# Kernel optimization log

Measured on AMD Instinct MI355X. Metric: run time of the kernel, lower is better.

Reference implementation:

```python
import jax, jax.numpy as jnp
import numpy as np

IN_FEATURES = 4096
OUT_FEATURES = 4096
SHARED_ROWS = 256
BATCH = 8192


def setup_inputs() -> dict:
    key = jax.random.key(0)
    k_x, k_w, k_b = jax.random.split(key, 3)
    x = jax.random.normal(k_x, (BATCH, IN_FEATURES), dtype=jnp.float32)
    shared_weights = jax.random.normal(k_w, (SHARED_ROWS, IN_FEATURES), dtype=jnp.float32)
    bias = jax.random.normal(k_b, (OUT_FEATURES,), dtype=jnp.float32)
    return {"x": x, "shared_weights": shared_weights, "bias": bias}


def reference(x, shared_weights, bias):
    # Faithful to torch: weight_matrix = shared_weights.repeat(out//shared, 1)
    reps = OUT_FEATURES // SHARED_ROWS
    weight_matrix = jnp.tile(shared_weights, (reps, 1))  # [out_features, in_features]
    # y = x @ W^T + b  -> [batch, out_features]
    return jnp.matmul(x, weight_matrix.T) + bias
```

## Files before the change

### kernel.cpp

```cpp
#include <hip/hip_runtime.h>
#include <cstdint>
#include <cstddef>

#define M_DIM 8192
#define N_DIM 256
#define K_DIM 4096
#define OUT_F 4096
#define BM 32
#define BK 64
#define NTH 512
#define LDK 72
#define S_LD 260

typedef float    float4_  __attribute__((ext_vector_type(4)));
typedef _Float16 half8    __attribute__((ext_vector_type(8)));
typedef _Float16 half4    __attribute__((ext_vector_type(4)));
typedef unsigned int uint4_ __attribute__((ext_vector_type(4)));

__global__ __launch_bounds__(256) void convert_w_kernel(const float* __restrict__ w,
                                                        _Float16* __restrict__ wh) {
  int i = (blockIdx.x * 256 + threadIdx.x) * 8;
  float4_ f0 = *(const float4_*)(w + i);
  float4_ f1 = *(const float4_*)(w + i + 4);
  half8 h;
  h[0] = (_Float16)f0[0]; h[1] = (_Float16)f0[1];
  h[2] = (_Float16)f0[2]; h[3] = (_Float16)f0[3];
  h[4] = (_Float16)f1[0]; h[5] = (_Float16)f1[1];
  h[6] = (_Float16)f1[2]; h[7] = (_Float16)f1[3];
  *(half8*)(wh + i) = h;
}

__global__ __launch_bounds__(512, 2) void swfc_kernel(const float* __restrict__ x,
                                                      const _Float16* __restrict__ wh,
                                                      const float* __restrict__ bias,
                                                      float* __restrict__ out) {
  __shared__ __align__(16) unsigned char smem[41472];
  _Float16 (*As)[LDK] = (_Float16(*)[LDK])smem;
  _Float16 (*Bs)[LDK] = (_Float16(*)[LDK])(smem + BM * LDK * 2);

  const int tid  = threadIdx.x;
  const int wv   = tid >> 6;
  const int lane = tid & 63;
  const int quad = lane >> 4;
  const int l16  = lane & 15;
  const int n0   = wv * 32;
  const int m0   = blockIdx.x * BM;

  const int arow = tid >> 4;
  const int acol = (tid & 15) * 4;
  const float* xg = x + (size_t)(m0 + arow) * K_DIM + acol;
  const int brow = tid >> 3;
  const int bcol = (tid & 7) * 8;
  const _Float16* wgb = wh + (size_t)brow * K_DIM + bcol;

  float4_ acc[2][2];
  const float4_ fzero = {0.f, 0.f, 0.f, 0.f};
#pragma unroll
  for (int i = 0; i < 2; ++i)
#pragma unroll
    for (int j = 0; j < 2; ++j) acc[i][j] = fzero;

  float4_ aPre = *(const float4_*)(xg);
  uint4_ bPre[4];
#pragma unroll
  for (int p = 0; p < 4; ++p)
    bPre[p] = *(const uint4_*)(wgb + (size_t)p * 64 * K_DIM);

  for (int kt = 0; kt < K_DIM / BK; ++kt) {
    half4 ah;
    ah[0] = (_Float16)aPre[0]; ah[1] = (_Float16)aPre[1];
    ah[2] = (_Float16)aPre[2]; ah[3] = (_Float16)aPre[3];
    *(half4*)(&As[arow][acol]) = ah;
#pragma unroll
    for (int p = 0; p < 4; ++p)
      *(uint4_*)(&Bs[p * 64 + brow][bcol]) = bPre[p];
    __syncthreads();

    if (kt < K_DIM / BK - 1) {
      const int k1 = (kt + 1) * BK;
      aPre = *(const float4_*)(xg + k1);
#pragma unroll
      for (int p = 0; p < 4; ++p)
        bPre[p] = *(const uint4_*)(wgb + (size_t)p * 64 * K_DIM + k1);
    }

#pragma unroll
    for (int ks = 0; ks < 2; ++ks) {
      const int koff = ks * 32 + quad * 8;
      half8 a0 = *(const half8*)(&As[l16][koff]);
      half8 a1 = *(const half8*)(&As[l16 + 16][koff]);
      half8 b0 = *(const half8*)(&Bs[n0 + l16][koff]);
      half8 b1 = *(const half8*)(&Bs[n0 + 16 + l16][koff]);
      acc[0][0] = __builtin_amdgcn_mfma_f32_16x16x32_f16(a0, b0, acc[0][0], 0, 0, 0);
      acc[1][0] = __builtin_amdgcn_mfma_f32_16x16x32_f16(a1, b0, acc[1][0], 0, 0, 0);
      acc[0][1] = __builtin_amdgcn_mfma_f32_16x16x32_f16(a0, b1, acc[0][1], 0, 0, 0);
      acc[1][1] = __builtin_amdgcn_mfma_f32_16x16x32_f16(a1, b1, acc[1][1], 0, 0, 0);
    }
    __syncthreads();
  }

  float* Sb = (float*)smem;
#pragma unroll
  for (int mf = 0; mf < 2; ++mf)
#pragma unroll
    for (int nf = 0; nf < 2; ++nf)
#pragma unroll
      for (int r = 0; r < 4; ++r)
        Sb[(mf * 16 + quad * 4 + r) * S_LD + n0 + nf * 16 + l16] = acc[mf][nf][r];
  __syncthreads();

  float4_ bv[2];
  const float4_* bias4 = (const float4_*)bias;
#pragma unroll
  for (int c = 0; c < 2; ++c) bv[c] = bias4[c * 512 + tid];

  const int sc = (tid & 63) * 4;
#pragma unroll 4
  for (int m = 0; m < BM; ++m) {
    float4_ s4 = *(const float4_*)(&Sb[m * S_LD + sc]);
    float4_* orow = (float4_*)(out + (size_t)(m0 + m) * OUT_F);
#pragma unroll
    for (int c = 0; c < 2; ++c) {
      orow[c * 512 + tid] = s4 + bv[c];
    }
  }
}

extern "C" void kernel_launch(void* const* d_in, const int* in_sizes, int n_in,
                              void* d_out, int out_size, void* d_ws, size_t ws_size,
                              hipStream_t stream) {
  const float* x    = (const float*)d_in[0];
  const float* w    = (const float*)d_in[1];
  const float* bias = (const float*)d_in[2];
  float* out        = (float*)d_out;
  _Float16* wh      = (_Float16*)d_ws;

  convert_w_kernel<<<(N_DIM * K_DIM) / (256 * 8), 256, 0, stream>>>(w, wh);
  swfc_kernel<<<M_DIM / BM, NTH, 0, stream>>>(x, wh, bias, out);
}
```

Baseline: 278.3 us.

## Split GEMM over K into workspace partials and add separate bias-expand kernel

The fused kernel is split in two. The first is a GEMM kernel with a larger 64-row tile, 8 accumulators per wave and split-K across blockIdx.y, which writes fp32 partial products of the 256 distinct output columns into workspace. The second, an expand kernel, sums the split-K partials, adds bias held in shared memory, and writes the 16 tiled copies to the output. The goal is more blocks in flight and more work per wave in the matmul. The cost is extra workspace traffic for the partials and an extra launch. The split factor depends on workspace size and drops to 1 when the workspace is small, which leaves only 128 GEMM blocks.

Measured after the change: 271.8 us. 2.3% less time.

```diff
diff --git a/kernel.cpp b/kernel.cpp
--- a/kernel.cpp
+++ b/kernel.cpp
@@ -6,11 +6,10 @@
 #define N_DIM 256
 #define K_DIM 4096
 #define OUT_F 4096
-#define BM 32
+#define BM 64
 #define BK 64
 #define NTH 512
 #define LDK 72
-#define S_LD 260
 
 typedef float    float4_  __attribute__((ext_vector_type(4)));
 typedef _Float16 half8    __attribute__((ext_vector_type(8)));
@@ -30,55 +29,58 @@
   *(half8*)(wh + i) = h;
 }
 
-__global__ __launch_bounds__(512, 2) void swfc_kernel(const float* __restrict__ x,
-                                                      const _Float16* __restrict__ wh,
-                                                      const float* __restrict__ bias,
-                                                      float* __restrict__ out) {
-  __shared__ __align__(16) unsigned char smem[41472];
-  _Float16 (*As)[LDK] = (_Float16(*)[LDK])smem;
-  _Float16 (*Bs)[LDK] = (_Float16(*)[LDK])(smem + BM * LDK * 2);
+__global__ __launch_bounds__(NTH, 4) void gemm_s_kernel(const float* __restrict__ x,
+                                                        const _Float16* __restrict__ wh,
+                                                        float* __restrict__ P,
+                                                        int nkt) {
+  __shared__ __align__(16) _Float16 As[BM][LDK];
+  __shared__ __align__(16) _Float16 Bs[N_DIM][LDK];
 
   const int tid  = threadIdx.x;
   const int wv   = tid >> 6;
   const int lane = tid & 63;
   const int quad = lane >> 4;
   const int l16  = lane & 15;
-  const int n0   = wv * 32;
+  const int mw   = wv >> 2;
+  const int n0   = (wv & 3) * 64;
   const int m0   = blockIdx.x * BM;
+  const int kbase = blockIdx.y * nkt * BK;
 
-  const int arow = tid >> 4;
-  const int acol = (tid & 15) * 4;
-  const float* xg = x + (size_t)(m0 + arow) * K_DIM + acol;
-  const int brow = tid >> 3;
-  const int bcol = (tid & 7) * 8;
-  const _Float16* wgb = wh + (size_t)brow * K_DIM + bcol;
+  const int arow = tid >> 3;
+  const int acol = (tid & 7) * 8;
+  const float* xg = x + (size_t)(m0 + arow) * K_DIM + kbase + acol;
+  const _Float16* wgb = wh + (size_t)arow * K_DIM + kbase + acol;
 
-  float4_ acc[2][2];
+  float4_ acc[2][4];
   const float4_ fzero = {0.f, 0.f, 0.f, 0.f};
 #pragma unroll
   for (int i = 0; i < 2; ++i)
 #pragma unroll
-    for (int j = 0; j < 2; ++j) acc[i][j] = fzero;
+    for (int j = 0; j < 4; ++j) acc[i][j] = fzero;
 
-  float4_ aPre = *(const float4_*)(xg);
+  float4_ aPre0 = *(const float4_*)(xg);
+  float4_ aPre1 = *(const float4_*)(xg + 4);
   uint4_ bPre[4];
 #pragma unroll
   for (int p = 0; p < 4; ++p)
     bPre[p] = *(const uint4_*)(wgb + (size_t)p * 64 * K_DIM);
 
-  for (int kt = 0; kt < K_DIM / BK; ++kt) {
-    half4 ah;
-    ah[0] = (_Float16)aPre[0]; ah[1] = (_Float16)aPre[1];
-    ah[2] = (_Float16)aPre[2]; ah[3] = (_Float16)aPre[3];
-    *(half4*)(&As[arow][acol]) = ah;
+  for (int kt = 0; kt < nkt; ++kt) {
+    half8 ah;
+    ah[0] = (_Float16)aPre0[0]; ah[1] = (_Float16)aPre0[1];
+    ah[2] = (_Float16)aPre0[2]; ah[3] = (_Float16)aPre0[3];
+    ah[4] = (_Float16)aPre1[0]; ah[5] = (_Float16)aPre1[1];
+    ah[6] = (_Float16)aPre1[2]; ah[7] = (_Float16)aPre1[3];
+    *(half8*)(&As[arow][acol]) = ah;
 #pragma unroll
     for (int p = 0; p < 4; ++p)
-      *(uint4_*)(&Bs[p * 64 + brow][bcol]) = bPre[p];
+      *(uint4_*)(&Bs[p * 64 + arow][acol]) = bPre[p];
     __syncthreads();
 
-    if (kt < K_DIM / BK - 1) {
+    if (kt + 1 < nkt) {
       const int k1 = (kt + 1) * BK;
-      aPre = *(const float4_*)(xg + k1);
+      aPre0 = *(const float4_*)(xg + k1);
+      aPre1 = *(const float4_*)(xg + k1 + 4);
 #pragma unroll
       for (int p = 0; p < 4; ++p)
         bPre[p] = *(const uint4_*)(wgb + (size_t)p * 64 * K_DIM + k1);
@@ -87,42 +89,62 @@
 #pragma unroll
     for (int ks = 0; ks < 2; ++ks) {
       const int koff = ks * 32 + quad * 8;
-      half8 a0 = *(const half8*)(&As[l16][koff]);
-      half8 a1 = *(const half8*)(&As[l16 + 16][koff]);
+      half8 a0 = *(const half8*)(&As[mw * 32 + l16][koff]);
+      half8 a1 = *(const half8*)(&As[mw * 32 + 16 + l16][koff]);
       half8 b0 = *(const half8*)(&Bs[n0 + l16][koff]);
       half8 b1 = *(const half8*)(&Bs[n0 + 16 + l16][koff]);
+      half8 b2 = *(const half8*)(&Bs[n0 + 32 + l16][koff]);
+      half8 b3 = *(const half8*)(&Bs[n0 + 48 + l16][koff]);
       acc[0][0] = __builtin_amdgcn_mfma_f32_16x16x32_f16(a0, b0, acc[0][0], 0, 0, 0);
       acc[1][0] = __builtin_amdgcn_mfma_f32_16x16x32_f16(a1, b0, acc[1][0], 0, 0, 0);
       acc[0][1] = __builtin_amdgcn_mfma_f32_16x16x32_f16(a0, b1, acc[0][1], 0, 0, 0);
       acc[1][1] = __builtin_amdgcn_mfma_f32_16x16x32_f16(a1, b1, acc[1][1], 0, 0, 0);
+      acc[0][2] = __builtin_amdgcn_mfma_f32_16x16x32_f16(a0, b2, acc[0][2], 0, 0, 0);
+      acc[1][2] = __builtin_amdgcn_mfma_f32_16x16x32_f16(a1, b2, acc[1][2], 0, 0, 0);
+      acc[0][3] = __builtin_amdgcn_mfma_f32_16x16x32_f16(a0, b3, acc[0][3], 0, 0, 0);
+      acc[1][3] = __builtin_amdgcn_mfma_f32_16x16x32_f16(a1, b3, acc[1][3], 0, 0, 0);
     }
     __syncthreads();
   }
 
-  float* Sb = (float*)smem;
+  float* Pout = P + (size_t)blockIdx.y * (M_DIM * N_DIM);
+  const int mbase = m0 + mw * 32 + quad * 4;
+  const int nbase = n0 + l16;
 #pragma unroll
   for (int mf = 0; mf < 2; ++mf)
 #pragma unroll
-    for (int nf = 0; nf < 2; ++nf)
+    for (int nf = 0; nf < 4; ++nf)
 #pragma unroll
       for (int r = 0; r < 4; ++r)
-        Sb[(mf * 16 + quad * 4 + r) * S_LD + n0 + nf * 16 + l16] = acc[mf][nf][r];
+        Pout[(size_t)(mbase + mf * 16 + r) * N_DIM + nbase + nf * 16] = acc[mf][nf][r];
+}
+
+__global__ __launch_bounds__(256) void expand_kernel(const float* __restrict__ P,
+                                                     const float* __restrict__ bias,
+                                                     float* __restrict__ out,
+                                                     int nks) {
+  __shared__ __align__(16) float bsh[OUT_F];
+  const int tid = threadIdx.x;
+  const float4_* b4 = (const float4_*)bias;
+  float4_* bs4 = (float4_*)bsh;
+#pragma unroll
+  for (int p = 0; p < 4; ++p) bs4[p * 256 + tid] = b4[p * 256 + tid];
   __syncthreads();
 
-  float4_ bv[2];
-  const float4_* bias4 = (const float4_*)bias;
+  const int ml  = tid >> 6;
+  const int c64 = tid & 63;
+  const float4_* P4 = (const float4_*)P;
+
 #pragma unroll
-  for (int c = 0; c < 2; ++c) bv[c] = bias4[c * 512 + tid];
-
-  const int sc = (tid & 63) * 4;
-#pragma unroll 4
-  for (int m = 0; m < BM; ++m) {
-    float4_ s4 = *(const float4_*)(&Sb[m * S_LD + sc]);
-    float4_* orow = (float4_*)(out + (size_t)(m0 + m) * OUT_F);
+  for (int pass = 0; pass < 2; ++pass) {
+    const int m = blockIdx.x * 8 + pass * 4 + ml;
+    float4_ s = {0.f, 0.f, 0.f, 0.f};
+    for (int ks = 0; ks < nks; ++ks)
+      s += P4[((size_t)ks * M_DIM + m) * (N_DIM / 4) + c64];
+    float4_* orow = (float4_*)(out + (size_t)m * OUT_F);
 #pragma unroll
-    for (int c = 0; c < 2; ++c) {
-      orow[c * 512 + tid] = s4 + bv[c];
-    }
+    for (int c = 0; c < 16; ++c)
+      orow[c * 64 + c64] = s + bs4[c * 64 + c64];
   }
 }
 
@@ -134,7 +156,15 @@
   const float* bias = (const float*)d_in[2];
   float* out        = (float*)d_out;
   _Float16* wh      = (_Float16*)d_ws;
+  float* P          = (float*)((char*)d_ws + (2u << 20));
+
+  const size_t whB    = (size_t)N_DIM * K_DIM * 2;
+  const size_t pslice = (size_t)M_DIM * N_DIM * 4;
+  int KS = (ws_size >= whB + 4 * pslice) ? 4
+         : (ws_size >= whB + 2 * pslice) ? 2 : 1;
+  int nkt = (K_DIM / BK) / KS;
 
   convert_w_kernel<<<(N_DIM * K_DIM) / (256 * 8), 256, 0, stream>>>(w, wh);
-  swfc_kernel<<<M_DIM / BM, NTH, 0, stream>>>(x, wh, bias, out);
+  gemm_s_kernel<<<dim3(M_DIM / BM, KS), NTH, 0, stream>>>(x, wh, P, nkt);
+  expand_kernel<<<M_DIM / 8, 256, 0, stream>>>(P, bias, out, KS);
 }
```
